# Kernel optimization log

Hardware: AMD Instinct MI355X
Metric: run time of the kernel (lower is better)

## Reference

```python
import jax, jax.numpy as jnp
import numpy as np

N, B, FIN, FOUT = 4096, 16, 128, 128
DENSITY = 0.01


def setup_inputs() -> dict:
    key = jax.random.key(0)
    k1, k2, k3, k4 = jax.random.split(key, 4)
    # sparse binary adjacency (static pattern), stored dense for the reference
    adj = (jax.random.uniform(k1, (N, N)) < DENSITY).astype(jnp.float32)
    x = jax.random.normal(k2, (B, N, FIN), dtype=jnp.float32)
    W = jax.random.normal(k3, (FOUT, FIN), dtype=jnp.float32) * (1.0 / np.sqrt(FIN))
    b = jax.random.normal(k4, (FOUT,), dtype=jnp.float32) * 0.01
    return {"adj": adj, "x": x, "W": W, "b": b}


def _normalized_adj(adj):
    # A_hat = D^{-1/2} (A + I) D^{-1/2}, degrees from column sums (dim=0 in torch)
    a_self = adj + jnp.eye(adj.shape[0], dtype=adj.dtype)
    dinv = jax.lax.rsqrt(jnp.sum(a_self, axis=0))
    return dinv[:, None] * a_self * dinv[None, :]


def reference(adj, x, W, b):
    a_norm = _normalized_adj(adj)
    # SpMM aggregation over nodes: (N,N) x (B,N,F) -> (B,N,F)
    agg = jnp.einsum('nm,bmf->bnf', a_norm, x)
    # dense linear transform: fc(agg)
    return jnp.einsum('bnf,of->bno', agg, W) + b
```

## Files before the change

kernel.cpp:

```cpp
#include <hip/hip_runtime.h>


#define NN 4096
#define FD 128
#define NB 16
#define CAP 96
#define CPAD 104
#define XB 512

typedef float     f32x4 __attribute__((ext_vector_type(4)));
typedef _Float16  f16x4 __attribute__((ext_vector_type(4)));
typedef _Float16  f16x8 __attribute__((ext_vector_type(8)));
typedef int       i32x2 __attribute__((ext_vector_type(2)));
typedef int       i32x4 __attribute__((ext_vector_type(4)));

#define XP 136

__device__ __forceinline__ float fmamix_lo(float acc, int pk, float w) {
    asm("v_fma_mix_f32 %0, %1, %2, %0 op_sel:[0,0,0] op_sel_hi:[1,0,0]"
        : "+v"(acc) : "v"(pk), "v"(w));
    return acc;
}
__device__ __forceinline__ float fmamix_hi(float acc, int pk, float w) {
    asm("v_fma_mix_f32 %0, %1, %2, %0 op_sel:[1,0,0] op_sel_hi:[1,0,0]"
        : "+v"(acc) : "v"(pk), "v"(w));
    return acc;
}

__global__ __launch_bounds__(256) void k_bx(const float* __restrict__ A,
                                            float* __restrict__ deg,
                                            int* __restrict__ cnt,
                                            unsigned short* __restrict__ csr,
                                            const float* __restrict__ x,
                                            const float* __restrict__ W,
                                            _Float16* __restrict__ y) {
    __shared__ __align__(16) char smem[FD * XP * 2];
    const int t = threadIdx.x;

    if (blockIdx.x < XB) {
        _Float16 (*sW)[XP] = (_Float16(*)[XP])smem;
        const size_t rbase = (size_t)blockIdx.x * 128;

        #pragma unroll
        for (int i = 0; i < 8; ++i) {
            const int id = t + i * 256;
            const int o = id >> 4, f8 = (id & 15) * 8;
            const f32x4 a = *(const f32x4*)&W[(size_t)o * FD + f8];
            const f32x4 b = *(const f32x4*)&W[(size_t)o * FD + f8 + 4];
            f16x8 h;
            h[0]=(_Float16)a.x; h[1]=(_Float16)a.y; h[2]=(_Float16)a.z; h[3]=(_Float16)a.w;
            h[4]=(_Float16)b.x; h[5]=(_Float16)b.y; h[6]=(_Float16)b.z; h[7]=(_Float16)b.w;
            *(f16x8*)&sW[o][f8] = h;
        }
        __syncthreads();

        const int w = t >> 6, lane = t & 63;
        const int lrow = lane & 15, koct = (lane >> 4) * 8;
        const float* xr0 = x + (rbase + w * 32 + lrow) * FD;
        const float* xr1 = xr0 + 16 * FD;
        f32x4 acc[2][8] = {};
        #pragma unroll
        for (int kc = 0; kc < 4; ++kc) {
            const int ko = kc * 32 + koct;
            const f32x4 a0 = *(const f32x4*)&xr0[ko];
            const f32x4 a1 = *(const f32x4*)&xr0[ko + 4];
            const f32x4 b0 = *(const f32x4*)&xr1[ko];
            const f32x4 b1 = *(const f32x4*)&xr1[ko + 4];
            f16x8 xx0, xx1;
            xx0[0]=(_Float16)a0.x; xx0[1]=(_Float16)a0.y; xx0[2]=(_Float16)a0.z; xx0[3]=(_Float16)a0.w;
            xx0[4]=(_Float16)a1.x; xx0[5]=(_Float16)a1.y; xx0[6]=(_Float16)a1.z; xx0[7]=(_Float16)a1.w;
            xx1[0]=(_Float16)b0.x; xx1[1]=(_Float16)b0.y; xx1[2]=(_Float16)b0.z; xx1[3]=(_Float16)b0.w;
            xx1[4]=(_Float16)b1.x; xx1[5]=(_Float16)b1.y; xx1[6]=(_Float16)b1.z; xx1[7]=(_Float16)b1.w;
            #pragma unroll
            for (int ot = 0; ot < 8; ++ot) {
                const f16x8 ww = *(const f16x8*)&sW[ot * 16 + lrow][ko];
                acc[0][ot] = __builtin_amdgcn_mfma_f32_16x16x32_f16(ww, xx0, acc[0][ot], 0, 0, 0);
                acc[1][ot] = __builtin_amdgcn_mfma_f32_16x16x32_f16(ww, xx1, acc[1][ot], 0, 0, 0);
            }
        }
        #pragma unroll
        for (int rt = 0; rt < 2; ++rt) {
            const size_t row = rbase + w * 32 + rt * 16 + (lane & 15);
            #pragma unroll
            for (int ot = 0; ot < 8; ++ot) {
                f16x4 h;
                h[0] = (_Float16)acc[rt][ot][0];
                h[1] = (_Float16)acc[rt][ot][1];
                h[2] = (_Float16)acc[rt][ot][2];
                h[3] = (_Float16)acc[rt][ot][3];
                *(f16x4*)&y[row * FD + ot * 16 + (lane >> 4) * 4] = h;
            }
        }
        return;
    }

    int* sWsum = (int*)smem;
    const int w = t >> 6, lane = t & 63;
    const int n0 = (blockIdx.x - XB) * 2;
    const float* row0 = A + (size_t)n0 * NN + t * 16;
    const float* row1 = row0 + NN;
    float r0[16], r1[16];
    *(f32x4*)&r0[0]  = ((const f32x4*)row0)[0];
    *(f32x4*)&r0[4]  = ((const f32x4*)row0)[1];
    *(f32x4*)&r0[8]  = ((const f32x4*)row0)[2];
    *(f32x4*)&r0[12] = ((const f32x4*)row0)[3];
    *(f32x4*)&r1[0]  = ((const f32x4*)row1)[0];
    *(f32x4*)&r1[4]  = ((const f32x4*)row1)[1];
    *(f32x4*)&r1[8]  = ((const f32x4*)row1)[2];
    *(f32x4*)&r1[12] = ((const f32x4*)row1)[3];

    int c0 = 0, c1 = 0;
    #pragma unroll
    for (int j = 0; j < 16; ++j) {
        c0 += (r0[j] != 0.0f) ? 1 : 0;
        c1 += (r1[j] != 0.0f) ? 1 : 0;
    }
    const int own = c0 | (c1 << 16);

    int s = own;
    #pragma unroll
    for (int off = 1; off < 64; off <<= 1) {
        const int u = __shfl(s, lane - off);
        s += (lane >= off) ? u : 0;
    }
    if (lane == 63) sWsum[w] = s;
    __syncthreads();
    int wbase = 0;
    #pragma unroll
    for (int j = 0; j < 4; ++j) wbase += (j < w) ? sWsum[j] : 0;

    const int base = wbase + s - own;
    int pos0 = base & 0xffff, pos1 = base >> 16;
    #pragma unroll
    for (int j = 0; j < 16; ++j) {
        const int m = t * 16 + j;
        if (r0[j] != 0.0f) {
            if (pos0 < CAP) csr[(size_t)n0 * CAP + pos0] = (unsigned short)m;
            ++pos0;
            atomicAdd(&deg[m], 1.0f);
        }
        if (r1[j] != 0.0f) {
            if (pos1 < CAP) csr[(size_t)(n0 + 1) * CAP + pos1] = (unsigned short)m;
            ++pos1;
            atomicAdd(&deg[m], 1.0f);
        }
    }
    if (t == 255) {
        const int tot = wbase + s;
        const int t0 = tot & 0xffff, t1 = tot >> 16;
        cnt[n0]     = t0 < CAP ? t0 : CAP;
        cnt[n0 + 1] = t1 < CAP ? t1 : CAP;
    }
}

__global__ __launch_bounds__(256) void k_agg2(const _Float16* __restrict__ y,
                                              const int* __restrict__ cnt,
                                              const unsigned short* __restrict__ csr,
                                              const float* __restrict__ deg,
                                              const float* __restrict__ bias,
                                              float* __restrict__ out) {
    __shared__ int sL[4][CPAD * 2];
    const int t = threadIdx.x, w = t >> 6, lane = t & 63;
    const int bid = blockIdx.x;
    const int xcd = bid & 7;
    const int b0  = 2 * xcd;
    const int n   = (bid >> 3) * 4 + w;
    const int c = cnt[n];
    const int totPad = (c + 1 + 3) & ~3;

    for (int k = lane; k < CPAD; k += 64) {
        int m; float wv;
        if (k < c)       { m = csr[(size_t)n * CAP + k]; wv = rsqrtf(1.0f + deg[m]); }
        else if (k == c) { m = n; wv = rsqrtf(1.0f + deg[n]); }
        else             { m = n; wv = 0.0f; }
        sL[w][2 * k]     = m << 8;
        sL[w][2 * k + 1] = __float_as_int(wv);
    }
    __syncthreads();

    const int rq = lane >> 4;
    const int fo = (lane & 15) * 16;
    const char* yb0 = (const char*)y + (size_t)b0 * (NN * FD * 2);
    const char* yb1 = yb0 + (size_t)(NN * FD * 2);

    float acc0[8] = {}, acc1[8] = {};
    #pragma unroll 2
    for (int k = rq; k < totPad; k += 4) {
        const i32x2 e = *(const i32x2*)&sL[w][2 * k];
        const unsigned v = (unsigned)(e.x + fo);
        const i32x4 pA = *(const i32x4*)(yb0 + v);
        const i32x4 pB = *(const i32x4*)(yb1 + v);
        const float wt = __int_as_float(e.y);
        #pragma unroll
        for (int j = 0; j < 4; ++j) {
            acc0[2*j]   = fmamix_lo(acc0[2*j],   pA[j], wt);
            acc0[2*j+1] = fmamix_hi(acc0[2*j+1], pA[j], wt);
            acc1[2*j]   = fmamix_lo(acc1[2*j],   pB[j], wt);
            acc1[2*j+1] = fmamix_hi(acc1[2*j+1], pB[j], wt);
        }
    }

    #pragma unroll
    for (int j = 0; j < 8; ++j) {
        acc0[j] += __shfl_xor(acc0[j], 16);
        acc0[j] += __shfl_xor(acc0[j], 32);
        acc1[j] += __shfl_xor(acc1[j], 16);
        acc1[j] += __shfl_xor(acc1[j], 32);
    }

    if (lane < 32) {
        const float dn = rsqrtf(1.0f + deg[n]);
        const int h = lane >> 4;
        const int f0 = (lane & 15) * 8 + h * 4;
        const f32x4 bb = *(const f32x4*)(bias + f0);
        f32x4 o0, o1;
        o0.x = acc0[h * 4 + 0] * dn + bb.x;
        o0.y = acc0[h * 4 + 1] * dn + bb.y;
        o0.z = acc0[h * 4 + 2] * dn + bb.z;
        o0.w = acc0[h * 4 + 3] * dn + bb.w;
        o1.x = acc1[h * 4 + 0] * dn + bb.x;
        o1.y = acc1[h * 4 + 1] * dn + bb.y;
        o1.z = acc1[h * 4 + 2] * dn + bb.z;
        o1.w = acc1[h * 4 + 3] * dn + bb.w;
        f32x4* d0 = (f32x4*)(out + ((size_t)b0 * NN + n) * FD + f0);
        f32x4* d1 = (f32x4*)(out + ((size_t)(b0 + 1) * NN + n) * FD + f0);
        __builtin_nontemporal_store(o0, d0);
        __builtin_nontemporal_store(o1, d1);
    }
}

extern "C" void kernel_launch(void* const* d_in, const int* in_sizes, int n_in,
                              void* d_out, int out_size, void* d_ws, size_t ws_size,
                              hipStream_t stream) {
    const float* A    = (const float*)d_in[0];
    const float* x    = (const float*)d_in[1];
    const float* W    = (const float*)d_in[2];
    const float* bias = (const float*)d_in[3];
    float* out = (float*)d_out;

    float*          deg  = (float*)d_ws;
    int*            cnt  = (int*)((char*)d_ws + 2 * NN * 4);
    unsigned short* csr  = (unsigned short*)(cnt + NN);
    _Float16*       y    = (_Float16*)((char*)d_ws + (3 * NN * 4 + (size_t)NN * CAP * 2));

    hipMemsetAsync(deg, 0, NN * sizeof(float), stream);
    k_bx  <<<XB + NN / 2, 256, 0, stream>>>(A, deg, cnt, csr, x, W, y);
    k_agg2<<<(NN / 4) * (NB / 2), 256, 0, stream>>>(y, cnt, csr, deg, bias, out);
}
```

Before: 76.59 us.

## Replace atomic degree counting with column-sum partial reduction blocks

Column degrees were counted with float atomicAdd per nonzero in the CSR-building blocks. They are now computed by 512 extra blocks that each sum a 128-row strip of the dense adjacency into a partial array, followed by a small kernel that reduces the 32 partials and precomputes rsqrt. This removes the atomics, the memset and the repeated rsqrt in the aggregation kernel. In exchange the 64 MB adjacency is read a second time (possibly from cache) and an extra kernel launch is added.

```diff
diff --git a/kernel.cpp b/kernel.cpp
--- a/kernel.cpp
+++ b/kernel.cpp
@@ -7,6 +7,7 @@
 #define CAP 96
 #define CPAD 104
 #define XB 512
+#define BB 2048
 
 typedef float     f32x4 __attribute__((ext_vector_type(4)));
 typedef _Float16  f16x4 __attribute__((ext_vector_type(4)));
@@ -28,7 +29,7 @@
 }
 
 __global__ __launch_bounds__(256) void k_bx(const float* __restrict__ A,
-                                            float* __restrict__ deg,
+                                            float* __restrict__ partial,
                                             int* __restrict__ cnt,
                                             unsigned short* __restrict__ csr,
                                             const float* __restrict__ x,
@@ -94,69 +95,89 @@
         return;
     }
 
-    int* sWsum = (int*)smem;
-    const int w = t >> 6, lane = t & 63;
-    const int n0 = (blockIdx.x - XB) * 2;
-    const float* row0 = A + (size_t)n0 * NN + t * 16;
-    const float* row1 = row0 + NN;
-    float r0[16], r1[16];
-    *(f32x4*)&r0[0]  = ((const f32x4*)row0)[0];
-    *(f32x4*)&r0[4]  = ((const f32x4*)row0)[1];
-    *(f32x4*)&r0[8]  = ((const f32x4*)row0)[2];
-    *(f32x4*)&r0[12] = ((const f32x4*)row0)[3];
-    *(f32x4*)&r1[0]  = ((const f32x4*)row1)[0];
-    *(f32x4*)&r1[4]  = ((const f32x4*)row1)[1];
-    *(f32x4*)&r1[8]  = ((const f32x4*)row1)[2];
-    *(f32x4*)&r1[12] = ((const f32x4*)row1)[3];
-
-    int c0 = 0, c1 = 0;
+    if (blockIdx.x < XB + BB) {
+        int* sWsum = (int*)smem;
+        const int w = t >> 6, lane = t & 63;
+        const int n0 = (blockIdx.x - XB) * 2;
+        const float* row0 = A + (size_t)n0 * NN + t * 16;
+        const float* row1 = row0 + NN;
+        float r0[16], r1[16];
+        *(f32x4*)&r0[0]  = ((const f32x4*)row0)[0];
+        *(f32x4*)&r0[4]  = ((const f32x4*)row0)[1];
+        *(f32x4*)&r0[8]  = ((const f32x4*)row0)[2];
+        *(f32x4*)&r0[12] = ((const f32x4*)row0)[3];
+        *(f32x4*)&r1[0]  = ((const f32x4*)row1)[0];
+        *(f32x4*)&r1[4]  = ((const f32x4*)row1)[1];
+        *(f32x4*)&r1[8]  = ((const f32x4*)row1)[2];
+        *(f32x4*)&r1[12] = ((const f32x4*)row1)[3];
+
+        int c0 = 0, c1 = 0;
+        #pragma unroll
+        for (int j = 0; j < 16; ++j) {
+            c0 += (r0[j] != 0.0f) ? 1 : 0;
+            c1 += (r1[j] != 0.0f) ? 1 : 0;
+        }
+        const int own = c0 | (c1 << 16);
+
+        int s = own;
+        #pragma unroll
+        for (int off = 1; off < 64; off <<= 1) {
+            const int u = __shfl(s, lane - off);
+            s += (lane >= off) ? u : 0;
+        }
+        if (lane == 63) sWsum[w] = s;
+        __syncthreads();
+        int wbase = 0;
+        #pragma unroll
+        for (int j = 0; j < 4; ++j) wbase += (j < w) ? sWsum[j] : 0;
+
+        const int base = wbase + s - own;
+        int pos0 = base & 0xffff, pos1 = base >> 16;
+        #pragma unroll
+        for (int j = 0; j < 16; ++j) {
+            const int m = t * 16 + j;
+            if (r0[j] != 0.0f) {
+                if (pos0 < CAP) csr[(size_t)n0 * CAP + pos0] = (unsigned short)m;
+                ++pos0;
+            }
+            if (r1[j] != 0.0f) {
+                if (pos1 < CAP) csr[(size_t)(n0 + 1) * CAP + pos1] = (unsigned short)m;
+                ++pos1;
+            }
+        }
+        if (t == 255) {
+            const int tot = wbase + s;
+            const int t0 = tot & 0xffff, t1 = tot >> 16;
+            cnt[n0]     = t0 < CAP ? t0 : CAP;
+            cnt[n0 + 1] = t1 < CAP ? t1 : CAP;
+        }
+        return;
+    }
+
+    const int q  = blockIdx.x - (XB + BB);
+    const int rb = q >> 4;
+    const int cb = q & 15;
+    const int c  = cb * 256 + t;
+    const float* p = A + (size_t)rb * 128 * NN + c;
+    float s = 0.0f;
+    #pragma unroll 8
+    for (int r = 0; r < 128; ++r) s += p[(size_t)r * NN];
+    partial[rb * NN + c] = s;
+}
+
+__global__ __launch_bounds__(256) void k_dinv2(const float* __restrict__ partial,
+                                               float* __restrict__ dinv) {
+    const int c = blockIdx.x * 256 + threadIdx.x;
+    float s = 1.0f;
     #pragma unroll
-    for (int j = 0; j < 16; ++j) {
-        c0 += (r0[j] != 0.0f) ? 1 : 0;
-        c1 += (r1[j] != 0.0f) ? 1 : 0;
-    }
-    const int own = c0 | (c1 << 16);
-
-    int s = own;
-    #pragma unroll
-    for (int off = 1; off < 64; off <<= 1) {
-        const int u = __shfl(s, lane - off);
-        s += (lane >= off) ? u : 0;
-    }
-    if (lane == 63) sWsum[w] = s;
-    __syncthreads();
-    int wbase = 0;
-    #pragma unroll
-    for (int j = 0; j < 4; ++j) wbase += (j < w) ? sWsum[j] : 0;
-
-    const int base = wbase + s - own;
-    int pos0 = base & 0xffff, pos1 = base >> 16;
-    #pragma unroll
-    for (int j = 0; j < 16; ++j) {
-        const int m = t * 16 + j;
-        if (r0[j] != 0.0f) {
-            if (pos0 < CAP) csr[(size_t)n0 * CAP + pos0] = (unsigned short)m;
-            ++pos0;
-            atomicAdd(&deg[m], 1.0f);
-        }
-        if (r1[j] != 0.0f) {
-            if (pos1 < CAP) csr[(size_t)(n0 + 1) * CAP + pos1] = (unsigned short)m;
-            ++pos1;
-            atomicAdd(&deg[m], 1.0f);
-        }
-    }
-    if (t == 255) {
-        const int tot = wbase + s;
-        const int t0 = tot & 0xffff, t1 = tot >> 16;
-        cnt[n0]     = t0 < CAP ? t0 : CAP;
-        cnt[n0 + 1] = t1 < CAP ? t1 : CAP;
-    }
+    for (int j = 0; j < 32; ++j) s += partial[j * NN + c];
+    dinv[c] = rsqrtf(s);
 }
 
 __global__ __launch_bounds__(256) void k_agg2(const _Float16* __restrict__ y,
                                               const int* __restrict__ cnt,
                                               const unsigned short* __restrict__ csr,
-                                              const float* __restrict__ deg,
+                                              const float* __restrict__ dinv,
                                               const float* __restrict__ bias,
                                               float* __restrict__ out) {
     __shared__ int sL[4][CPAD * 2];
@@ -170,8 +191,8 @@
 
     for (int k = lane; k < CPAD; k += 64) {
         int m; float wv;
-        if (k < c)       { m = csr[(size_t)n * CAP + k]; wv = rsqrtf(1.0f + deg[m]); }
-        else if (k == c) { m = n; wv = rsqrtf(1.0f + deg[n]); }
+        if (k < c)       { m = csr[(size_t)n * CAP + k]; wv = dinv[m]; }
+        else if (k == c) { m = n; wv = dinv[n]; }
         else             { m = n; wv = 0.0f; }
         sL[w][2 * k]     = m << 8;
         sL[w][2 * k + 1] = __float_as_int(wv);
@@ -209,7 +230,7 @@
     }
 
     if (lane < 32) {
-        const float dn = rsqrtf(1.0f + deg[n]);
+        const float dn = dinv[n];
         const int h = lane >> 4;
         const int f0 = (lane & 15) * 8 + h * 4;
         const f32x4 bb = *(const f32x4*)(bias + f0);
@@ -238,12 +259,13 @@
     const float* bias = (const float*)d_in[3];
     float* out = (float*)d_out;
 
-    float*          deg  = (float*)d_ws;
-    int*            cnt  = (int*)((char*)d_ws + 2 * NN * 4);
-    unsigned short* csr  = (unsigned short*)(cnt + NN);
-    _Float16*       y    = (_Float16*)((char*)d_ws + (3 * NN * 4 + (size_t)NN * CAP * 2));
-
-    hipMemsetAsync(deg, 0, NN * sizeof(float), stream);
-    k_bx  <<<XB + NN / 2, 256, 0, stream>>>(A, deg, cnt, csr, x, W, y);
-    k_agg2<<<(NN / 4) * (NB / 2), 256, 0, stream>>>(y, cnt, csr, deg, bias, out);
-}
+    float*          partial = (float*)d_ws;
+    float*          dinv    = partial + 32 * NN;
+    int*            cnt     = (int*)(dinv + NN);
+    unsigned short* csr     = (unsigned short*)(cnt + NN);
+    _Float16*       y       = (_Float16*)((char*)csr + (size_t)NN * CAP * 2);
+
+    k_bx   <<<XB + BB + 512, 256, 0, stream>>>(A, partial, cnt, csr, x, W, y);
+    k_dinv2<<<NN / 256, 256, 0, stream>>>(partial, dinv);
+    k_agg2 <<<(NN / 4) * (NB / 2), 256, 0, stream>>>(y, cnt, csr, dinv, bias, out);
+}
```

After: 79.06 us. +3.2%, slower.
